# Performance work log

Measured on AMD Instinct MI355X. Metric: run time of the kernel, lower is better.

The kernel has to match this reference:

```python
import jax, jax.numpy as jnp
import numpy as np


def setup_inputs() -> dict:
    key = jax.random.key(0)
    k1, k2, k3, k4 = jax.random.split(key, 4)
    B, T, C, H, W = 16, 8, 1024, 14, 14
    x = jax.random.normal(k1, (B * T, C, H, W), dtype=jnp.float32)
    # learned spectral filter, stored as real/imag pairs: [T, H, W, C//2+1, 2]
    wfilt = jax.random.normal(k2, (T, H, W, C // 2 + 1, 2), dtype=jnp.float32) * 0.02
    # 1x1x1 Conv3d over channels -> plain [out, in] matrix + bias
    conv_w = jax.random.normal(k3, (C, C), dtype=jnp.float32) * (1.0 / np.sqrt(C))
    conv_b = jax.random.normal(k4, (C,), dtype=jnp.float32) * 0.01
    return {"x": x, "wfilt": wfilt, "conv_w": conv_w, "conv_b": conv_b, "n_segments": T}


def reference(x, wfilt, conv_w, conv_b, n_segments):
    bt, c, h, w = x.shape
    t = n_segments
    b = bt // t
    x5 = x.reshape(b, t, c, h, w)
    # move channels last: [b, t, h, w, c]
    d = jnp.transpose(x5, (0, 1, 3, 4, 2))
    # rFFT along channel axis, ortho norm
    f = jnp.fft.rfft(d, axis=4, norm="ortho")  # [b, t, h, w, c//2+1]
    wc = jax.lax.complex(wfilt[..., 0], wfilt[..., 1])  # [t, h, w, c//2+1]
    f = f * wc  # broadcast over batch
    d = jnp.fft.irfft(f, n=c, axis=4, norm="ortho")  # [b, t, h, w, c]
    d = jnp.transpose(d, (0, 1, 4, 2, 3))  # [b, t, c, h, w]
    # enhancement: 1x1x1 Conv3d over channels + exact GELU
    e = jnp.einsum("btchw,oc->btohw", d, conv_w) + conv_b[None, None, :, None, None]
    e = jax.nn.gelu(e, approximate=False)
    return (x5 + e).reshape(bt, c, h, w)
```

## Files before the change

kernel.cpp:

```cpp
#include <hip/hip_runtime.h>
#include <hip/hip_bf16.h>
#include <math.h>

typedef short short8 __attribute__((ext_vector_type(8)));
typedef float f32x4 __attribute__((ext_vector_type(4)));

#define BTN   128
#define HWN   196
#define CCH   1024
#define NPIX  (BTN * HWN)
#define BTSTR (CCH * HWN)

#define WS_D  0
#define WS_BW 51380224

__device__ __forceinline__ float2 cadd(float2 a, float2 b) { return make_float2(a.x + b.x, a.y + b.y); }
__device__ __forceinline__ float2 csub(float2 a, float2 b) { return make_float2(a.x - b.x, a.y - b.y); }
__device__ __forceinline__ float2 cmulf(float2 a, float2 b) {
  return make_float2(a.x * b.x - a.y * b.y, a.x * b.y + a.y * b.x);
}
__device__ __forceinline__ float2 cmulc(float2 a, float2 b) {
  return make_float2(a.x * b.x + a.y * b.y, a.y * b.x - a.x * b.y);
}
__device__ __forceinline__ float2 csqr(float2 a) {
  return make_float2(a.x * a.x - a.y * a.y, 2.f * a.x * a.y);
}
__device__ __forceinline__ float2 cneg(float2 a) { return make_float2(-a.x, -a.y); }
__device__ __forceinline__ unsigned short f2bf(float f) {
  unsigned u = __float_as_uint(f);
  unsigned r = (u + 0x7fffu + ((u >> 16) & 1u)) >> 16;
  return (unsigned short)r;
}

__global__ void wcast_kernel(const float* __restrict__ w, unsigned short* __restrict__ o) {
  int i = (blockIdx.x * 256 + threadIdx.x) * 4;
  float4 v = *(const float4*)(w + i);
  uint2 u;
  u.x = (unsigned)f2bf(v.x) | ((unsigned)f2bf(v.y) << 16);
  u.y = (unsigned)f2bf(v.z) | ((unsigned)f2bf(v.w) << 16);
  *(uint2*)(o + i) = u;
}

#define TS 1088

__global__ __launch_bounds__(256) void fft_filter_kernel(
    const float* __restrict__ x, const float* __restrict__ wfilt,
    unsigned short* __restrict__ dmat) {
  __shared__ float tile[8 * TS];
  __shared__ float2 tw10s[257];
  int tid = threadIdx.x;
  int l = tid & 63, w = tid >> 6;

  for (int i = tid; i < 257; i += 256) {
    float s, c;
    __sincosf(-6.283185307179586f * (float)i / 1024.0f, &s, &c);
    tw10s[i] = make_float2(c, s);
  }

  int blk = (blockIdx.x & 7) * 392 + (blockIdx.x >> 3);
  int p_base = blk * 8;

  {
    int g = tid & 1, chb = tid >> 1;
    int p = p_base + 4 * g;
    int bt = p / HWN, hw = p - bt * HWN;
    const float* src = x + (size_t)bt * BTSTR + hw;
    float* rowb = tile + (4 * g) * TS;
#pragma unroll
    for (int it = 0; it < 8; ++it) {
      int c = chb + 128 * it;
      float4 v = *(const float4*)(src + (size_t)c * HWN);
      float* b = rowb + c;
      b[0 * TS] = v.x; b[1 * TS] = v.y; b[2 * TS] = v.z; b[3 * TS] = v.w;
    }
  }
  __syncthreads();

  const float H = 0.70710678118654752f;
  float2 Wl;
  { float s, c; __sincosf(-6.283185307179586f * (float)l / 512.0f, &s, &c); Wl = make_float2(c, s); }
  float2 W2l = csqr(Wl), W4l = csqr(W2l);
  float2 W2li = make_float2(W2l.y, -W2l.x);
  float2 T01 = cmulf(Wl, make_float2(H, -H));
  float2 T02 = make_float2(Wl.y, -Wl.x);
  float2 T03 = cmulf(Wl, make_float2(-H, -H));
  float2 t3 = csqr(W4l); if (l & 32) t3 = cneg(t3);
  float2 t4 = csqr(t3);  if (l & 16) t4 = cneg(t4);
  float2 t5 = csqr(t4);  if (l & 8)  t5 = cneg(t5);
  float2 t6 = csqr(t5);  if (l & 4)  t6 = cneg(t6);
  float2 t7 = csqr(t6);  if (l & 2)  t7 = cneg(t7);

  int pA = p_base + 2 * w, pB = pA + 1;
  int btA = pA / HWN, hwA = pA - btA * HWN;
  int btB = pB / HWN, hwB = pB - btB * HWN;
  float2* rowA = (float2*)(tile + (2 * w) * TS);
  float2* rowB = (float2*)(tile + (2 * w + 1) * TS);

  float2 z[2][8];
#pragma unroll
  for (int r = 0; r < 8; ++r) { z[0][r] = rowA[l + 64 * r]; z[1][r] = rowB[l + 64 * r]; }

  {
    float2 T0[4] = {Wl, T01, T02, T03};
#pragma unroll
    for (int q = 0; q < 2; ++q)
#pragma unroll
      for (int r = 0; r < 4; ++r) {
        float2 a = z[q][r], b = z[q][r + 4];
        z[q][r] = cadd(a, b);
        z[q][r + 4] = cmulf(csub(a, b), T0[r]);
      }
  }
#pragma unroll
  for (int q = 0; q < 2; ++q)
#pragma unroll
    for (int h = 0; h < 2; ++h) {
      int b0 = h * 4;
      float2 a = z[q][b0], b = z[q][b0 + 2];
      z[q][b0] = cadd(a, b); z[q][b0 + 2] = cmulf(csub(a, b), W2l);
      a = z[q][b0 + 1]; b = z[q][b0 + 3];
      z[q][b0 + 1] = cadd(a, b); z[q][b0 + 3] = cmulf(csub(a, b), W2li);
    }
#pragma unroll
  for (int q = 0; q < 2; ++q)
#pragma unroll
    for (int r = 0; r < 8; r += 2) {
      float2 a = z[q][r], b = z[q][r + 1];
      z[q][r] = cadd(a, b); z[q][r + 1] = cmulf(csub(a, b), W4l);
    }
  {
    float2 tws[6] = {t3, t4, t5, t6, t7, make_float2(1.f, 0.f)};
    int masks[6] = {32, 16, 8, 4, 2, 1};
#pragma unroll
    for (int s = 0; s < 6; ++s) {
      int m = masks[s];
      bool up = (l & m) != 0;
      float2 te = up ? tws[s] : make_float2(1.f, 0.f);
#pragma unroll
      for (int r = 0; r < 8; ++r)
#pragma unroll
        for (int q = 0; q < 2; ++q) {
          float2 v = z[q][r];
          float2 o = make_float2(__shfl_xor(v.x, m, 64), __shfl_xor(v.y, m, 64));
          float2 d = up ? csub(o, v) : cadd(v, o);
          z[q][r] = cmulf(d, te);
        }
    }
  }

#pragma unroll
  for (int r = 0; r < 8; ++r) {
    int pidx = l + (l >> 4) + 68 * r;
    rowA[pidx] = z[0][r]; rowB[pidx] = z[1][r];
  }
  {
    const float* wfA = wfilt + (size_t)((btA & 7) * HWN + hwA) * 1026;
    const float* wfB = wfilt + (size_t)((btB & 7) * HWN + hwB) * 1026;
    const float sc = 1.0f / 512.0f;
#pragma unroll
    for (int i = 0; i < 4; ++i) {
      int f = 64 * i + l;
      if (f == 0) {
        {
          float2 z0 = rowA[0];
          float X0 = z0.x + z0.y, X512 = z0.x - z0.y;
          float Y0 = X0 * wfA[0] * sc;
          float Y512 = X512 * wfA[1024] * sc;
          rowA[0] = make_float2(0.5f * (Y0 + Y512), 0.5f * (Y0 - Y512));
          float2 z2 = rowA[1];
          float2 X256 = make_float2(z2.x, -z2.y);
          float2 Y = cmulf(X256, make_float2(wfA[512], wfA[513]));
          rowA[1] = make_float2(Y.x * sc, -Y.y * sc);
        }
        {
          float2 z0 = rowB[0];
          float X0 = z0.x + z0.y, X512 = z0.x - z0.y;
          float Y0 = X0 * wfB[0] * sc;
          float Y512 = X512 * wfB[1024] * sc;
          rowB[0] = make_float2(0.5f * (Y0 + Y512), 0.5f * (Y0 - Y512));
          float2 z2 = rowB[1];
          float2 X256 = make_float2(z2.x, -z2.y);
          float2 Y = cmulf(X256, make_float2(wfB[512], wfB[513]));
          rowB[1] = make_float2(Y.x * sc, -Y.y * sc);
        }
      } else {
        int g = 512 - f;
        int pf = (int)(__brev((unsigned)f) >> 23);
        int pg = (int)(__brev((unsigned)g) >> 23);
        int pf2 = pf + (pf >> 4), pg2 = pg + (pg >> 4);
        float2 Wf = tw10s[f];
        float2 Wfc = make_float2(Wf.x, -Wf.y);
#pragma unroll
        for (int q = 0; q < 2; ++q) {
          float2* zq = q ? rowB : rowA;
          const float* wf = q ? wfB : wfA;
          float2 Zf = zq[pf2], Zg = zq[pg2];
          float2 A = make_float2(0.5f * (Zf.x + Zg.x), 0.5f * (Zf.y - Zg.y));
          float2 B = make_float2(0.5f * (Zf.y + Zg.y), -0.5f * (Zf.x - Zg.x));
          float2 WB = cmulf(Wf, B);
          float2 Xf = make_float2(A.x + WB.x, A.y + WB.y);
          float2 Xg = make_float2(A.x - WB.x, -(A.y - WB.y));
          float2 Yf = cmulf(Xf, make_float2(wf[2 * f], wf[2 * f + 1]));
          float2 Yg = cmulf(Xg, make_float2(wf[2 * g], wf[2 * g + 1]));
          Yf.x *= sc; Yf.y *= sc; Yg.x *= sc; Yg.y *= sc;
          float2 Ap = make_float2(0.5f * (Yf.x + Yg.x), 0.5f * (Yf.y - Yg.y));
          float2 T  = make_float2(0.5f * (Yf.x - Yg.x), 0.5f * (Yf.y + Yg.y));
          float2 Bp = cmulf(Wfc, T);
          zq[pf2] = make_float2(Ap.x - Bp.y, Ap.y + Bp.x);
          zq[pg2] = make_float2(Ap.x + Bp.y, Bp.x - Ap.y);
        }
      }
    }
  }
#pragma unroll
  for (int r = 0; r < 8; ++r) {
    int pidx = l + (l >> 4) + 68 * r;
    z[0][r] = rowA[pidx]; z[1][r] = rowB[pidx];
  }

  {
    float2 tws[6] = {make_float2(1.f, 0.f), t7, t6, t5, t4, t3};
    int masks[6] = {1, 2, 4, 8, 16, 32};
#pragma unroll
    for (int s = 0; s < 6; ++s) {
      int m = masks[s];
      bool up = (l & m) != 0;
      float2 te = up ? make_float2(tws[s].x, -tws[s].y) : make_float2(1.f, 0.f);
#pragma unroll
      for (int r = 0; r < 8; ++r)
#pragma unroll
        for (int q = 0; q < 2; ++q) {
          float2 v = cmulf(z[q][r], te);
          float2 o = make_float2(__shfl_xor(v.x, m, 64), __shfl_xor(v.y, m, 64));
          z[q][r] = up ? csub(o, v) : cadd(v, o);
        }
    }
  }
#pragma unroll
  for (int q = 0; q < 2; ++q)
#pragma unroll
    for (int r = 0; r < 8; r += 2) {
      float2 v = cmulc(z[q][r + 1], W4l);
      float2 a = z[q][r];
      z[q][r] = cadd(a, v); z[q][r + 1] = csub(a, v);
    }
#pragma unroll
  for (int q = 0; q < 2; ++q)
#pragma unroll
    for (int h = 0; h < 2; ++h) {
      int b0 = h * 4;
      float2 v = cmulc(z[q][b0 + 2], W2l);
      float2 a = z[q][b0];
      z[q][b0] = cadd(a, v); z[q][b0 + 2] = csub(a, v);
      v = cmulc(z[q][b0 + 3], W2li);
      a = z[q][b0 + 1];
      z[q][b0 + 1] = cadd(a, v); z[q][b0 + 3] = csub(a, v);
    }
  {
    float2 T0[4] = {Wl, T01, T02, T03};
#pragma unroll
    for (int q = 0; q < 2; ++q)
#pragma unroll
      for (int r = 0; r < 4; ++r) {
        float2 v = cmulc(z[q][r + 4], T0[r]);
        float2 a = z[q][r];
        z[q][r] = cadd(a, v); z[q][r + 4] = csub(a, v);
      }
  }

  unsigned* dstA = (unsigned*)(dmat + (size_t)pA * CCH);
  unsigned* dstB = (unsigned*)(dmat + (size_t)pB * CCH);
#pragma unroll
  for (int r = 0; r < 8; ++r) {
    float2 vA = z[0][r], vB = z[1][r];
    dstA[l + 64 * r] = (unsigned)f2bf(vA.x) | ((unsigned)f2bf(vA.y) << 16);
    dstB[l + 64 * r] = (unsigned)f2bf(vB.x) | ((unsigned)f2bf(vB.y) << 16);
  }
}

#define GLOAD16(gsrc, ldst)                                                     \
  __builtin_amdgcn_global_load_lds(                                             \
      (const __attribute__((address_space(1))) unsigned int*)(gsrc),            \
      (__attribute__((address_space(3))) unsigned int*)(ldst), 16, 0, 0)

__global__ __launch_bounds__(512) void gemm_gelu_kernel(
    const unsigned short* __restrict__ A,
    const unsigned short* __restrict__ Bw,
    const float* __restrict__ bias,
    const float* __restrict__ x,
    float* __restrict__ out) {
  __shared__ unsigned short SH[24576];
  unsigned short* lA = SH;
  unsigned short* lB = SH + 12288;

  int bid = blockIdx.x;
  int j = (bid & 7) * 196 + (bid >> 3);
  int mt = j >> 3, nt = j & 7;
  int p0 = mt * 128, n0 = nt * 128;

  int tid = threadIdx.x;
  int l = tid & 63, wid = tid >> 6;
  int wr = wid >> 2, wc = wid & 3;
  int lr = l & 15, lg = l >> 4;

  f32x4 acc[2][4];
#pragma unroll
  for (int i = 0; i < 2; ++i)
#pragma unroll
    for (int jj = 0; jj < 4; ++jj) acc[i][jj] = f32x4{0.f, 0.f, 0.f, 0.f};

  int arow = tid >> 2;
  int acg = (tid & 3) ^ ((tid >> 3) & 3);
  const unsigned short* agA = A  + (size_t)(p0 + arow) * CCH + acg * 8;
  const unsigned short* agB = Bw + (size_t)(n0 + arow) * CCH + acg * 8;
  unsigned short* laW = lA + wid * 512;
  unsigned short* lbW = lB + wid * 512;

  int kx = ((lg ^ ((lr >> 1) & 3)) << 3);
  const unsigned short* lAf0 = lA + (wr * 64 + lr) * 32 + kx;
  const unsigned short* lBf0 = lB + (wc * 32 + lr) * 32 + kx;

#define STAGE(buf, kt)                                                          \
  do {                                                                          \
    GLOAD16(agA + (kt) * 32, laW + (buf) * 4096);                               \
    GLOAD16(agB + (kt) * 32, lbW + (buf) * 4096);                               \
  } while (0)

  STAGE(0, 0);
  STAGE(1, 1);
  __builtin_amdgcn_sched_barrier(0);

  int brd = 0, bst = 2;
#pragma unroll 2
  for (int kk = 0; kk < 32; ++kk) {
    asm volatile("s_waitcnt vmcnt(2)" ::: "memory");
    __builtin_amdgcn_s_barrier();
    __builtin_amdgcn_sched_barrier(0);

    STAGE(bst, (kk + 2) & 31);

    short8 af[4], bf[2];
    const unsigned short* lAf = lAf0 + brd * 4096;
    const unsigned short* lBf = lBf0 + brd * 4096;
#pragma unroll
    for (int m = 0; m < 4; ++m) af[m] = *(const short8*)(lAf + m * 512);
#pragma unroll
    for (int n = 0; n < 2; ++n) bf[n] = *(const short8*)(lBf + n * 512);
    __builtin_amdgcn_s_setprio(1);
#pragma unroll
    for (int i = 0; i < 2; ++i)
#pragma unroll
      for (int jj = 0; jj < 4; ++jj)
        acc[i][jj] = __builtin_amdgcn_mfma_f32_16x16x32_bf16(bf[i], af[jj], acc[i][jj], 0, 0, 0);
    __builtin_amdgcn_s_setprio(0);
    __builtin_amdgcn_sched_barrier(0);

    brd = (brd == 2) ? 0 : brd + 1;
    bst = (bst == 2) ? 0 : bst + 1;
  }
#undef STAGE
  asm volatile("s_waitcnt vmcnt(0)" ::: "memory");
  __syncthreads();

  float* tp = (float*)SH + wid * 544;
  int pxb = p0 + wr * 64 + (l & 15) * 4;
  int btE = pxb / HWN, hwE = pxb - btE * HWN;
  size_t ebase = (size_t)btE * BTSTR + hwE;

#pragma unroll
  for (int i = 0; i < 2; ++i) {
#pragma unroll
    for (int rr = 0; rr < 2; ++rr) {
#pragma unroll
      for (int jj = 0; jj < 4; ++jj) {
#pragma unroll
        for (int s = 0; s < 2; ++s)
          tp[(lg * 2 + s) * 68 + jj * 16 + lr] = acc[i][jj][2 * rr + s];
      }
      asm volatile("s_waitcnt lgkmcnt(0)" ::: "memory");
      __builtin_amdgcn_sched_barrier(0);
#pragma unroll
      for (int cb = 0; cb < 8; cb += 4) {
        int ct = cb + (l >> 4);
        f32x4 v4 = *(const f32x4*)(tp + ct * 68 + (l & 15) * 4);
        int ch = n0 + wc * 32 + i * 16 + ((ct >> 1) << 2) + 2 * rr + (ct & 1);
        size_t idx = ebase + (size_t)ch * HWN;
        float4 xv = *(const float4*)(x + idx);
        float bc = bias[ch];
        float4 ov;
        {
          float v0 = v4[0] + bc, v1 = v4[1] + bc, v2 = v4[2] + bc, v3 = v4[3] + bc;
          ov.x = xv.x + 0.5f * v0 * (1.0f + erff(v0 * 0.70710678118654752f));
          ov.y = xv.y + 0.5f * v1 * (1.0f + erff(v1 * 0.70710678118654752f));
          ov.z = xv.z + 0.5f * v2 * (1.0f + erff(v2 * 0.70710678118654752f));
          ov.w = xv.w + 0.5f * v3 * (1.0f + erff(v3 * 0.70710678118654752f));
        }
        *(float4*)(out + idx) = ov;
      }
      __builtin_amdgcn_sched_barrier(0);
    }
  }
}

extern "C" void kernel_launch(void* const* d_in, const int* in_sizes, int n_in,
                              void* d_out, int out_size, void* d_ws, size_t ws_size,
                              hipStream_t stream) {
  const float* x      = (const float*)d_in[0];
  const float* wfilt  = (const float*)d_in[1];
  const float* conv_w = (const float*)d_in[2];
  const float* conv_b = (const float*)d_in[3];
  char* ws = (char*)d_ws;
  unsigned short* dmat = (unsigned short*)(ws + WS_D);
  unsigned short* bw   = (unsigned short*)(ws + WS_BW);
  float* out           = (float*)d_out;

  wcast_kernel<<<1024, 256, 0, stream>>>(conv_w, bw);
  fft_filter_kernel<<<3136, 256, 0, stream>>>(x, wfilt, dmat);
  gemm_gelu_kernel<<<1568, 512, 0, stream>>>(dmat, bw, conv_b, x, out);
}
```

Before: 170.1 us.

## Load GEMM weight fragments straight into registers, bypassing LDS staging

The weight (B) operand of the GELU GEMM is now loaded from global memory straight into MFMA register fragments with register double-buffering, instead of staging through LDS. The k-loop is manually unrolled by two to ping-pong the register buffers. Only the activation (A) tiles remain in a triple-buffered LDS pipeline, which halves LDS use and may allow more resident blocks. In exchange, weight rows are fetched redundantly by each wave row, and the vmcnt wait counts become harder to get right.

```diff
diff --git a/kernel.cpp b/kernel.cpp
--- a/kernel.cpp
+++ b/kernel.cpp
@@ -289,9 +289,7 @@
     const float* __restrict__ bias,
     const float* __restrict__ x,
     float* __restrict__ out) {
-  __shared__ unsigned short SH[24576];
-  unsigned short* lA = SH;
-  unsigned short* lB = SH + 12288;
+  __shared__ unsigned short SH[12288];
 
   int bid = blockIdx.x;
   int j = (bid & 7) * 196 + (bid >> 3);
@@ -311,54 +309,77 @@
 
   int arow = tid >> 2;
   int acg = (tid & 3) ^ ((tid >> 3) & 3);
-  const unsigned short* agA = A  + (size_t)(p0 + arow) * CCH + acg * 8;
-  const unsigned short* agB = Bw + (size_t)(n0 + arow) * CCH + acg * 8;
-  unsigned short* laW = lA + wid * 512;
-  unsigned short* lbW = lB + wid * 512;
+  const unsigned short* agA = A + (size_t)(p0 + arow) * CCH + acg * 8;
+  unsigned short* laW = SH + wid * 512;
 
   int kx = ((lg ^ ((lr >> 1) & 3)) << 3);
-  const unsigned short* lAf0 = lA + (wr * 64 + lr) * 32 + kx;
-  const unsigned short* lBf0 = lB + (wc * 32 + lr) * 32 + kx;
-
-#define STAGE(buf, kt)                                                          \
+  const unsigned short* lAf0 = SH + (wr * 64 + lr) * 32 + kx;
+
+  const unsigned short* bgW = Bw + (size_t)(n0 + wc * 32 + lr) * CCH + lg * 8;
+
+#define STAGE_A(buf, kt) GLOAD16(agA + (kt) * 32, laW + (buf) * 4096)
+#define LOADB(dst, kt)                                                          \
   do {                                                                          \
-    GLOAD16(agA + (kt) * 32, laW + (buf) * 4096);                               \
-    GLOAD16(agB + (kt) * 32, lbW + (buf) * 4096);                               \
+    dst[0] = *(const short8*)(bgW + (kt) * 32);                                 \
+    dst[1] = *(const short8*)(bgW + (size_t)16 * CCH + (kt) * 32);              \
   } while (0)
-
-  STAGE(0, 0);
-  STAGE(1, 1);
+#define READ_AF(af, b)                                                          \
+  do {                                                                          \
+    const unsigned short* lAf = lAf0 + (b) * 4096;                              \
+    _Pragma("unroll") for (int m = 0; m < 4; ++m)                               \
+      af[m] = *(const short8*)(lAf + m * 512);                                  \
+  } while (0)
+#define DO_MFMA(bfr, af)                                                        \
+  do {                                                                          \
+    __builtin_amdgcn_s_setprio(1);                                              \
+    _Pragma("unroll") for (int i = 0; i < 2; ++i)                               \
+      _Pragma("unroll") for (int jj = 0; jj < 4; ++jj)                          \
+        acc[i][jj] = __builtin_amdgcn_mfma_f32_16x16x32_bf16(bfr[i], af[jj],    \
+                                                             acc[i][jj], 0, 0, 0); \
+    __builtin_amdgcn_s_setprio(0);                                              \
+  } while (0)
+
+  short8 bA[2], bB[2];
+  LOADB(bA, 0);
+  STAGE_A(0, 0);
+  STAGE_A(1, 1);
   __builtin_amdgcn_sched_barrier(0);
 
   int brd = 0, bst = 2;
-#pragma unroll 2
-  for (int kk = 0; kk < 32; ++kk) {
-    asm volatile("s_waitcnt vmcnt(2)" ::: "memory");
+#pragma unroll 1
+  for (int kk = 0; kk < 32; kk += 2) {
+    asm volatile("s_waitcnt vmcnt(1)" ::: "memory");
     __builtin_amdgcn_s_barrier();
     __builtin_amdgcn_sched_barrier(0);
-
-    STAGE(bst, (kk + 2) & 31);
-
-    short8 af[4], bf[2];
-    const unsigned short* lAf = lAf0 + brd * 4096;
-    const unsigned short* lBf = lBf0 + brd * 4096;
-#pragma unroll
-    for (int m = 0; m < 4; ++m) af[m] = *(const short8*)(lAf + m * 512);
-#pragma unroll
-    for (int n = 0; n < 2; ++n) bf[n] = *(const short8*)(lBf + n * 512);
-    __builtin_amdgcn_s_setprio(1);
-#pragma unroll
-    for (int i = 0; i < 2; ++i)
-#pragma unroll
-      for (int jj = 0; jj < 4; ++jj)
-        acc[i][jj] = __builtin_amdgcn_mfma_f32_16x16x32_bf16(bf[i], af[jj], acc[i][jj], 0, 0, 0);
-    __builtin_amdgcn_s_setprio(0);
+    LOADB(bB, kk + 1);
+    STAGE_A(bst, (kk + 2) & 31);
+    bst = (bst == 2) ? 0 : bst + 1;
+    {
+      short8 af[4];
+      READ_AF(af, brd);
+      brd = (brd == 2) ? 0 : brd + 1;
+      DO_MFMA(bA, af);
+    }
     __builtin_amdgcn_sched_barrier(0);
 
-    brd = (brd == 2) ? 0 : brd + 1;
+    asm volatile("s_waitcnt vmcnt(1)" ::: "memory");
+    __builtin_amdgcn_s_barrier();
+    __builtin_amdgcn_sched_barrier(0);
+    LOADB(bA, (kk + 2) & 31);
+    STAGE_A(bst, (kk + 3) & 31);
     bst = (bst == 2) ? 0 : bst + 1;
-  }
-#undef STAGE
+    {
+      short8 af[4];
+      READ_AF(af, brd);
+      brd = (brd == 2) ? 0 : brd + 1;
+      DO_MFMA(bB, af);
+    }
+    __builtin_amdgcn_sched_barrier(0);
+  }
+#undef STAGE_A
+#undef LOADB
+#undef READ_AF
+#undef DO_MFMA
   asm volatile("s_waitcnt vmcnt(0)" ::: "memory");
   __syncthreads();
 
```

Result: slower. 221.9 us (+30.5%).
